# Optimization experiments

Measured on AMD Instinct MI355X. Metric: run time of the kernel, lower is better.

Reference implementation:

```python
import jax, jax.numpy as jnp
import numpy as np

N_MOLS = 2048       # number of molecules (segments)
BOND_FDIM = 14      # slice last BOND_FDIM columns of f_bonds
DEPTH = 3


def setup_inputs() -> dict:
    key = jax.random.key(0)
    ks = jax.random.split(key, 12)
    n_atoms, n_bonds = 65536, 131072
    atom_fdim, bond_total, hidden, max_nb = 133, 147, 256, 6
    atom_features = jax.random.normal(ks[0], (n_atoms, atom_fdim), jnp.float32)
    f_bonds = jax.random.normal(ks[1], (n_bonds, bond_total), jnp.float32)
    a2a = jax.random.randint(ks[2], (n_atoms, max_nb), 0, n_atoms, jnp.int32)
    a2b = jax.random.randint(ks[3], (n_atoms, max_nb), 0, n_bonds, jnp.int32)
    segment_ids = jnp.sort(jax.random.randint(ks[4], (n_atoms,), 0, N_MOLS, jnp.int32))
    s = 0.05
    Wi = jax.random.normal(ks[5], (atom_fdim, hidden), jnp.float32) * s
    bi = jax.random.normal(ks[6], (hidden,), jnp.float32) * s
    Wh = jax.random.normal(ks[7], (hidden + BOND_FDIM, hidden), jnp.float32) * s
    bh = jax.random.normal(ks[8], (hidden,), jnp.float32) * s
    Wo = jax.random.normal(ks[9], (atom_fdim + hidden, hidden), jnp.float32) * s
    bo = jax.random.normal(ks[10], (hidden,), jnp.float32) * s
    return {"atom_features": atom_features, "f_bonds": f_bonds, "a2a": a2a,
            "a2b": a2b, "segment_ids": segment_ids,
            "Wi": Wi, "bi": bi, "Wh": Wh, "bh": bh, "Wo": Wo, "bo": bo}


def reference(atom_features, f_bonds, a2a, a2b, segment_ids, Wi, bi, Wh, bh, Wo, bo):
    # W_i + ReLU
    inp = atom_features @ Wi + bi                      # [N, H]
    message = jax.nn.relu(inp)
    fb = f_bonds[:, -BOND_FDIM:]                       # slice last bond_fdim cols
    # depth-1 message passing steps
    for _ in range(DEPTH - 1):
        nei_a_sum = message[a2a].sum(axis=1)           # [N, H]   gather + sum
        nei_b_sum = fb[a2b].sum(axis=1)                # [N, Fb]  gather + sum
        # sum(concat) == concat(sums) over neighbor axis
        m = jnp.concatenate([nei_a_sum, nei_b_sum], axis=1) @ Wh + bh
        message = jax.nn.relu(inp + m)                 # dropout: eval mode (identity)
    # final atom readout
    a_message = message[a2a].sum(axis=1)               # [N, H]
    a_input = jnp.concatenate([atom_features, a_message], axis=1)
    atom_hiddens = jax.nn.relu(a_input @ Wo + bo)      # [N, H]
    # segment-mean pooling over molecules (empty segments -> zero vector)
    sums = jax.ops.segment_sum(atom_hiddens, segment_ids, num_segments=N_MOLS)
    counts = jax.ops.segment_sum(jnp.ones((atom_hiddens.shape[0],), atom_hiddens.dtype),
                                 segment_ids, num_segments=N_MOLS)
    vecs = jnp.where(counts[:, None] > 0, sums / jnp.maximum(counts, 1.0)[:, None], 0.0)
    return vecs
```

## Files before the change

kernel.cpp:

```cpp
#include <hip/hip_runtime.h>

#define N_ATOMS 65536
#define AF      133
#define BT      147
#define HID     256
#define NNB     6
#define NM      2048

#define KI   160
#define KB   32
#define KP   256
#define LSI  168
#define LSB  40
#define LSP  264

typedef __attribute__((ext_vector_type(8))) short short8;
typedef __attribute__((ext_vector_type(4))) float f32x4;

__device__ __forceinline__ unsigned short f2bf(float f) {
    unsigned u = __builtin_bit_cast(unsigned, f);
    u += 0x7fffu + ((u >> 16) & 1u);
    return (unsigned short)(u >> 16);
}
__device__ __forceinline__ float bf2f(unsigned short s) {
    unsigned u = ((unsigned)s) << 16;
    return __builtin_bit_cast(float, u);
}

__global__ __launch_bounds__(256) void k_prep_bond(const float* __restrict__ Wi,
                                                   const float* __restrict__ Wh,
                                                   const float* __restrict__ Wo,
                                                   const float* __restrict__ bi,
                                                   const float* __restrict__ bh,
                                                   const float* __restrict__ f_bonds,
                                                   const int* __restrict__ a2b,
                                                   unsigned short* __restrict__ Wi_t,
                                                   unsigned short* __restrict__ Wb_t,
                                                   unsigned short* __restrict__ Whm_t,
                                                   unsigned short* __restrict__ Woa_t,
                                                   unsigned short* __restrict__ Wom_t,
                                                   unsigned short* __restrict__ bondsum,
                                                   float* __restrict__ b_ih) {
    if (blockIdx.x < 256) {
        const int n = blockIdx.x;
        if (n == 0) b_ih[threadIdx.x] = bi[threadIdx.x] + bh[threadIdx.x];
        for (int k = threadIdx.x; k < KI; k += 256) {
            Wi_t[n * KI + k]  = f2bf(k < AF ? Wi[k * HID + n] : 0.f);
            Woa_t[n * KI + k] = f2bf(k < AF ? Wo[k * HID + n] : 0.f);
        }
        for (int k = threadIdx.x; k < KB; k += 256)
            Wb_t[n * KB + k] = f2bf(k < 14 ? Wh[(HID + k) * HID + n] : 0.f);
        for (int k = threadIdx.x; k < KP; k += 256) {
            Whm_t[n * KP + k] = f2bf(Wh[k * HID + n]);
            Wom_t[n * KP + k] = f2bf(Wo[(AF + k) * HID + n]);
        }
    } else {
        const int id   = (blockIdx.x - 256) * 256 + threadIdx.x;
        const int atom = id >> 4;
        const int c    = id & 15;
        float s = 0.f;
        if (c < 14) {
            const int* nb = &a2b[atom * NNB];
#pragma unroll
            for (int t = 0; t < NNB; ++t)
                s += f_bonds[(size_t)nb[t] * BT + (BT - 14) + c];
        }
        bondsum[atom * 32 + c]      = f2bf(s);
        bondsum[atom * 32 + 16 + c] = 0;
    }
}

template<int K, int LS>
__device__ __forceinline__ void mfma_core(const unsigned short* __restrict__ As,
                                          const unsigned short* __restrict__ Wt,
                                          f32x4 (&acc)[2][4], int wave, int lane) {
    const int lm = lane & 15, quad = lane >> 4;
    for (int ks = 0; ks < K; ks += 32) {
        short8 af[2], bf[4];
#pragma unroll
        for (int rt = 0; rt < 2; ++rt)
            af[rt] = *(const short8*)&As[(rt * 16 + lm) * LS + ks + quad * 8];
#pragma unroll
        for (int ct = 0; ct < 4; ++ct)
            bf[ct] = *(const short8*)&Wt[(size_t)(wave * 64 + ct * 16 + lm) * K + ks + quad * 8];
#pragma unroll
        for (int rt = 0; rt < 2; ++rt)
#pragma unroll
            for (int ct = 0; ct < 4; ++ct)
                acc[rt][ct] = __builtin_amdgcn_mfma_f32_16x16x32_bf16(af[rt], bf[ct], acc[rt][ct], 0, 0, 0);
    }
}

template<int K, int LS>
__device__ __forceinline__ void mfma_core2(const unsigned short* __restrict__ As,
                                           const unsigned short* __restrict__ WtA,
                                           const unsigned short* __restrict__ WtB,
                                           f32x4 (&accA)[2][4], f32x4 (&accB)[2][4],
                                           int wave, int lane) {
    const int lm = lane & 15, quad = lane >> 4;
    for (int ks = 0; ks < K; ks += 32) {
        short8 af[2], bfA[4], bfB[4];
#pragma unroll
        for (int rt = 0; rt < 2; ++rt)
            af[rt] = *(const short8*)&As[(rt * 16 + lm) * LS + ks + quad * 8];
#pragma unroll
        for (int ct = 0; ct < 4; ++ct) {
            size_t off = (size_t)(wave * 64 + ct * 16 + lm) * K + ks + quad * 8;
            bfA[ct] = *(const short8*)&WtA[off];
            bfB[ct] = *(const short8*)&WtB[off];
        }
#pragma unroll
        for (int rt = 0; rt < 2; ++rt)
#pragma unroll
            for (int ct = 0; ct < 4; ++ct) {
                accA[rt][ct] = __builtin_amdgcn_mfma_f32_16x16x32_bf16(af[rt], bfA[ct], accA[rt][ct], 0, 0, 0);
                accB[rt][ct] = __builtin_amdgcn_mfma_f32_16x16x32_bf16(af[rt], bfB[ct], accB[rt][ct], 0, 0, 0);
            }
    }
}

__device__ __forceinline__ void epi_to_lds(f32x4 (&acc)[2][4],
                                           const float* __restrict__ bias,
                                           bool relu_,
                                           unsigned short* __restrict__ E,
                                           int wave, int lane) {
    const int lm = lane & 15, quad = lane >> 4;
#pragma unroll
    for (int ct = 0; ct < 4; ++ct) {
        int col = wave * 64 + ct * 16 + lm;
        float bv = bias ? bias[col] : 0.f;
#pragma unroll
        for (int rt = 0; rt < 2; ++rt)
#pragma unroll
            for (int i = 0; i < 4; ++i) {
                float v = acc[rt][ct][i] + bv;
                if (relu_) v = fmaxf(v, 0.f);
                E[(rt * 16 + quad * 4 + i) * LSP + col] = f2bf(v);
            }
    }
}

__device__ __forceinline__ void store_tile32(unsigned short* __restrict__ dst, int base,
                                             const unsigned short* __restrict__ E, int tid) {
#pragma unroll
    for (int k = 0; k < 4; ++k) {
        int j = k * 256 + tid;
        int r = j >> 5, g = j & 31;
        *(short8*)&dst[(size_t)(base + r) * HID + g * 8] = *(const short8*)&E[r * LSP + g * 8];
    }
}

__global__ __launch_bounds__(256, 4) void k_inp(const float* __restrict__ atom,
                                                const unsigned short* __restrict__ bondsum,
                                                const unsigned short* __restrict__ Wi_t,
                                                const unsigned short* __restrict__ Wb_t,
                                                const unsigned short* __restrict__ Whm_t,
                                                const unsigned short* __restrict__ Woa_t,
                                                const float* __restrict__ bi,
                                                const float* __restrict__ b_ih,
                                                const float* __restrict__ bo,
                                                unsigned short* __restrict__ P0,
                                                unsigned short* __restrict__ inp2,
                                                unsigned short* __restrict__ aw) {
    __shared__ unsigned short atomT[32 * LSI];
    __shared__ unsigned short work[32 * LSP];
    __shared__ unsigned short bs[32 * LSB];
    const int tid  = threadIdx.x;
    const int base = blockIdx.x * 32;

    for (int it = tid; it < 32 * KI; it += 256) {
        int r = it / KI, c = it - r * KI;
        atomT[r * LSI + c] = f2bf(c < AF ? atom[(size_t)(base + r) * AF + c] : 0.f);
    }
    if (tid < 128) {
        int r = tid >> 2, c = (tid & 3) * 8;
        *(short8*)&bs[r * LSB + c] = *(const short8*)&bondsum[(size_t)(base + r) * 32 + c];
    }
    __syncthreads();

    const int lane = tid & 63, wave = tid >> 6;
    f32x4 acc1[2][4] = {}, acc3[2][4] = {};
    mfma_core2<KI, LSI>(atomT, Wi_t, Woa_t, acc1, acc3, wave, lane);

    epi_to_lds(acc3, bo, false, work, wave, lane);
    __syncthreads();
    store_tile32(aw, base, work, tid);
    __syncthreads();

    epi_to_lds(acc1, bi, true, work, wave, lane);
    __syncthreads();

    f32x4 acc2[2][4] = {};
    mfma_core<KP, LSP>(work, Whm_t, acc2, wave, lane);
    mfma_core<KB, LSB>(bs, Wb_t, acc1, wave, lane);
    __syncthreads();

    epi_to_lds(acc2, nullptr, false, work, wave, lane);
    __syncthreads();
    store_tile32(P0, base, work, tid);
    __syncthreads();
    epi_to_lds(acc1, b_ih, false, work, wave, lane);
    __syncthreads();
    store_tile32(inp2, base, work, tid);
}

__global__ __launch_bounds__(256, 6) void k_it(const unsigned short* __restrict__ Pin,
                                               const unsigned short* __restrict__ base_,
                                               const int* __restrict__ a2a,
                                               const unsigned short* __restrict__ Wt,
                                               unsigned short* __restrict__ Pout) {
    __shared__ unsigned short mT[32 * LSP];
    __shared__ int nb_l[32 * NNB];
    const int tid  = threadIdx.x;
    const int base = blockIdx.x * 32;

    if (tid < 32 * NNB) nb_l[tid] = a2a[base * NNB + tid];
    __syncthreads();

#pragma unroll 1
    for (int k = 0; k < 4; ++k) {
        int j = k * 256 + tid;
        int r = j >> 5, g = j & 31;
        const int* nb = &nb_l[r * NNB];
        float s[8] = {};
#pragma unroll
        for (int t = 0; t < NNB; ++t) {
            short8 u = *(const short8*)&Pin[(size_t)nb[t] * HID + g * 8];
#pragma unroll
            for (int q = 0; q < 8; ++q) s[q] += bf2f((unsigned short)u[q]);
        }
        short8 b = *(const short8*)&base_[(size_t)(base + r) * HID + g * 8];
        short8 o;
#pragma unroll
        for (int q = 0; q < 8; ++q)
            o[q] = (short)f2bf(fmaxf(s[q] + bf2f((unsigned short)b[q]), 0.f));
        *(short8*)&mT[r * LSP + g * 8] = o;
    }
    __syncthreads();

    const int lane = tid & 63, wave = tid >> 6;
    f32x4 acc[2][4] = {};
    mfma_core<KP, LSP>(mT, Wt, acc, wave, lane);
    __syncthreads();
    epi_to_lds(acc, nullptr, false, mT, wave, lane);
    __syncthreads();
    store_tile32(Pout, base, mT, tid);
}

__global__ __launch_bounds__(256, 6) void k_gseg(const unsigned short* __restrict__ P,
                                                 const unsigned short* __restrict__ aw,
                                                 const int* __restrict__ a2a,
                                                 const int* __restrict__ seg,
                                                 float* __restrict__ out) {
    const int m = blockIdx.x;
    __shared__ int lohi[2];
    __shared__ float red[8 * 256];
    if (threadIdx.x == 0) {
        int lo = 0, hi = N_ATOMS;
        while (lo < hi) { int mid = (lo + hi) >> 1; if (seg[mid] < m) lo = mid + 1; else hi = mid; }
        lohi[0] = lo;
        int lo2 = lo, hi2 = N_ATOMS;
        while (lo2 < hi2) { int mid = (lo2 + hi2) >> 1; if (seg[mid] < m + 1) lo2 = mid + 1; else hi2 = mid; }
        lohi[1] = lo2;
    }
    __syncthreads();
    const int lo = lohi[0], hi = lohi[1];
    const int slot = threadIdx.x >> 5;
    const int cg   = threadIdx.x & 31;

    float s[8] = {};
#pragma unroll 1
    for (int i0 = lo; i0 < hi; i0 += 8) {
        int i = i0 + slot;
        if (i < hi) {
            const int* nb = &a2a[i * NNB];
            short8 a = *(const short8*)&aw[(size_t)i * HID + cg * 8];
            float v[8];
#pragma unroll
            for (int q = 0; q < 8; ++q) v[q] = bf2f((unsigned short)a[q]);
#pragma unroll
            for (int t = 0; t < NNB; ++t) {
                short8 u = *(const short8*)&P[(size_t)nb[t] * HID + cg * 8];
#pragma unroll
                for (int q = 0; q < 8; ++q) v[q] += bf2f((unsigned short)u[q]);
            }
#pragma unroll
            for (int q = 0; q < 8; ++q) s[q] += fmaxf(v[q], 0.f);
        }
    }
#pragma unroll
    for (int q = 0; q < 8; ++q) red[slot * 256 + cg * 8 + q] = s[q];
    __syncthreads();

    const int j = threadIdx.x;
    float tot = 0.f;
#pragma unroll
    for (int sl = 0; sl < 8; ++sl) tot += red[sl * 256 + j];
    const int cnt = hi - lo;
    out[m * HID + j] = (cnt > 0) ? (tot / (float)cnt) : 0.f;
}

extern "C" void kernel_launch(void* const* d_in, const int* in_sizes, int n_in,
                              void* d_out, int out_size, void* d_ws, size_t ws_size,
                              hipStream_t stream) {
    const float* atom    = (const float*)d_in[0];
    const float* f_bonds = (const float*)d_in[1];
    const int*   a2a     = (const int*)d_in[2];
    const int*   a2b     = (const int*)d_in[3];
    const int*   seg     = (const int*)d_in[4];
    const float* Wi      = (const float*)d_in[5];
    const float* bi      = (const float*)d_in[6];
    const float* Wh      = (const float*)d_in[7];
    const float* bh      = (const float*)d_in[8];
    const float* Wo      = (const float*)d_in[9];
    const float* bo      = (const float*)d_in[10];
    float* out = (float*)d_out;

    unsigned short* ws = (unsigned short*)d_ws;
    const size_t nh = (size_t)N_ATOMS * HID;
    unsigned short* Pa   = ws;
    unsigned short* Pb   = Pa + nh;
    unsigned short* inp2 = Pb + nh;
    unsigned short* aw   = inp2 + nh;
    unsigned short* bsum = aw + nh;
    unsigned short* Wi_t  = bsum + (size_t)N_ATOMS * 32;
    unsigned short* Wb_t  = Wi_t + 256 * KI;
    unsigned short* Whm_t = Wb_t + 256 * KB;
    unsigned short* Woa_t = Whm_t + 256 * KP;
    unsigned short* Wom_t = Woa_t + 256 * KI;
    float*          b_ih  = (float*)(Wom_t + 256 * KP);

    dim3 blk(256);
    const int nb32 = N_ATOMS / 32;

    k_prep_bond<<<256 + N_ATOMS * 16 / 256, blk, 0, stream>>>(
        Wi, Wh, Wo, bi, bh, f_bonds, a2b,
        Wi_t, Wb_t, Whm_t, Woa_t, Wom_t, bsum, b_ih);
    k_inp<<<nb32, blk, 0, stream>>>(atom, bsum, Wi_t, Wb_t, Whm_t, Woa_t,
                                    bi, b_ih, bo, Pa, inp2, aw);

    k_it<<<nb32, blk, 0, stream>>>(Pa, inp2, a2a, Whm_t, Pb);
    k_it<<<nb32, blk, 0, stream>>>(Pb, inp2, a2a, Wom_t, Pa);
    k_gseg<<<NM, blk, 0, stream>>>(Pa, aw, a2a, seg, out);
}
```

Before: 374.7 us.

## Pre-swizzle weights into MFMA fragment order and reduce k_inp barriers

Weights are now written in an MFMA-fragment-ordered layout, so each lane loads its B fragment as one contiguous short8 and a wave reads fully coalesced 1KB chunks instead of strided rows. The K loops are fully unrolled. In k_inp the shared buffers are pooled so the atom tile buffer is reused as a second epilogue buffer, which lets two epilogues and two stores share one barrier and removes several __syncthreads. This costs extra index math in the prep kernel and more register pressure from unrolling.

Result: faster. 329.1 us (-12.2%).

```diff
diff --git a/kernel.cpp b/kernel.cpp
--- a/kernel.cpp
+++ b/kernel.cpp
@@ -25,6 +25,11 @@
 __device__ __forceinline__ float bf2f(unsigned short s) {
     unsigned u = ((unsigned)s) << 16;
     return __builtin_bit_cast(float, u);
+}
+
+__device__ __forceinline__ size_t fidx(int K, int n, int k) {
+    return ((size_t)(((n >> 4) * (K >> 5) + (k >> 5)) * 64
+                     + (((k >> 3) & 3) << 4) + (n & 15)) << 3) + (k & 7);
 }
 
 __global__ __launch_bounds__(256) void k_prep_bond(const float* __restrict__ Wi,
@@ -34,25 +39,25 @@
                                                    const float* __restrict__ bh,
                                                    const float* __restrict__ f_bonds,
                                                    const int* __restrict__ a2b,
-                                                   unsigned short* __restrict__ Wi_t,
-                                                   unsigned short* __restrict__ Wb_t,
-                                                   unsigned short* __restrict__ Whm_t,
-                                                   unsigned short* __restrict__ Woa_t,
-                                                   unsigned short* __restrict__ Wom_t,
+                                                   unsigned short* __restrict__ Wi_f,
+                                                   unsigned short* __restrict__ Wb_f,
+                                                   unsigned short* __restrict__ Whm_f,
+                                                   unsigned short* __restrict__ Woa_f,
+                                                   unsigned short* __restrict__ Wom_f,
                                                    unsigned short* __restrict__ bondsum,
                                                    float* __restrict__ b_ih) {
     if (blockIdx.x < 256) {
         const int n = blockIdx.x;
         if (n == 0) b_ih[threadIdx.x] = bi[threadIdx.x] + bh[threadIdx.x];
         for (int k = threadIdx.x; k < KI; k += 256) {
-            Wi_t[n * KI + k]  = f2bf(k < AF ? Wi[k * HID + n] : 0.f);
-            Woa_t[n * KI + k] = f2bf(k < AF ? Wo[k * HID + n] : 0.f);
+            Wi_f[fidx(KI, n, k)]  = f2bf(k < AF ? Wi[k * HID + n] : 0.f);
+            Woa_f[fidx(KI, n, k)] = f2bf(k < AF ? Wo[k * HID + n] : 0.f);
         }
         for (int k = threadIdx.x; k < KB; k += 256)
-            Wb_t[n * KB + k] = f2bf(k < 14 ? Wh[(HID + k) * HID + n] : 0.f);
+            Wb_f[fidx(KB, n, k)] = f2bf(k < 14 ? Wh[(HID + k) * HID + n] : 0.f);
         for (int k = threadIdx.x; k < KP; k += 256) {
-            Whm_t[n * KP + k] = f2bf(Wh[k * HID + n]);
-            Wom_t[n * KP + k] = f2bf(Wo[(AF + k) * HID + n]);
+            Whm_f[fidx(KP, n, k)] = f2bf(Wh[k * HID + n]);
+            Wom_f[fidx(KP, n, k)] = f2bf(Wo[(AF + k) * HID + n]);
         }
     } else {
         const int id   = (blockIdx.x - 256) * 256 + threadIdx.x;
@@ -75,14 +80,16 @@
                                           const unsigned short* __restrict__ Wt,
                                           f32x4 (&acc)[2][4], int wave, int lane) {
     const int lm = lane & 15, quad = lane >> 4;
-    for (int ks = 0; ks < K; ks += 32) {
+    const short8* __restrict__ Wf = (const short8*)Wt;
+#pragma unroll
+    for (int ks = 0; ks < (K >> 5); ++ks) {
         short8 af[2], bf[4];
 #pragma unroll
         for (int rt = 0; rt < 2; ++rt)
-            af[rt] = *(const short8*)&As[(rt * 16 + lm) * LS + ks + quad * 8];
+            af[rt] = *(const short8*)&As[(rt * 16 + lm) * LS + ks * 32 + quad * 8];
 #pragma unroll
         for (int ct = 0; ct < 4; ++ct)
-            bf[ct] = *(const short8*)&Wt[(size_t)(wave * 64 + ct * 16 + lm) * K + ks + quad * 8];
+            bf[ct] = Wf[(size_t)((wave * 4 + ct) * (K >> 5) + ks) * 64 + lane];
 #pragma unroll
         for (int rt = 0; rt < 2; ++rt)
 #pragma unroll
@@ -98,16 +105,19 @@
                                            f32x4 (&accA)[2][4], f32x4 (&accB)[2][4],
                                            int wave, int lane) {
     const int lm = lane & 15, quad = lane >> 4;
-    for (int ks = 0; ks < K; ks += 32) {
+    const short8* __restrict__ WfA = (const short8*)WtA;
+    const short8* __restrict__ WfB = (const short8*)WtB;
+#pragma unroll
+    for (int ks = 0; ks < (K >> 5); ++ks) {
         short8 af[2], bfA[4], bfB[4];
 #pragma unroll
         for (int rt = 0; rt < 2; ++rt)
-            af[rt] = *(const short8*)&As[(rt * 16 + lm) * LS + ks + quad * 8];
+            af[rt] = *(const short8*)&As[(rt * 16 + lm) * LS + ks * 32 + quad * 8];
 #pragma unroll
         for (int ct = 0; ct < 4; ++ct) {
-            size_t off = (size_t)(wave * 64 + ct * 16 + lm) * K + ks + quad * 8;
-            bfA[ct] = *(const short8*)&WtA[off];
-            bfB[ct] = *(const short8*)&WtB[off];
+            size_t off = (size_t)((wave * 4 + ct) * (K >> 5) + ks) * 64 + lane;
+            bfA[ct] = WfA[off];
+            bfB[ct] = WfB[off];
         }
 #pragma unroll
         for (int rt = 0; rt < 2; ++rt)
@@ -152,25 +162,26 @@
 
 __global__ __launch_bounds__(256, 4) void k_inp(const float* __restrict__ atom,
                                                 const unsigned short* __restrict__ bondsum,
-                                                const unsigned short* __restrict__ Wi_t,
-                                                const unsigned short* __restrict__ Wb_t,
-                                                const unsigned short* __restrict__ Whm_t,
-                                                const unsigned short* __restrict__ Woa_t,
+                                                const unsigned short* __restrict__ Wi_f,
+                                                const unsigned short* __restrict__ Wb_f,
+                                                const unsigned short* __restrict__ Whm_f,
+                                                const unsigned short* __restrict__ Woa_f,
                                                 const float* __restrict__ bi,
                                                 const float* __restrict__ b_ih,
                                                 const float* __restrict__ bo,
                                                 unsigned short* __restrict__ P0,
                                                 unsigned short* __restrict__ inp2,
                                                 unsigned short* __restrict__ aw) {
-    __shared__ unsigned short atomT[32 * LSI];
-    __shared__ unsigned short work[32 * LSP];
-    __shared__ unsigned short bs[32 * LSB];
+    __shared__ unsigned short pool[8448 + 8448 + 1280];
+    unsigned short* X    = pool;
+    unsigned short* work = pool + 8448;
+    unsigned short* bs   = pool + 16896;
     const int tid  = threadIdx.x;
     const int base = blockIdx.x * 32;
 
     for (int it = tid; it < 32 * KI; it += 256) {
         int r = it / KI, c = it - r * KI;
-        atomT[r * LSI + c] = f2bf(c < AF ? atom[(size_t)(base + r) * AF + c] : 0.f);
+        X[r * LSI + c] = f2bf(c < AF ? atom[(size_t)(base + r) * AF + c] : 0.f);
     }
     if (tid < 128) {
         int r = tid >> 2, c = (tid & 3) * 8;
@@ -180,27 +191,24 @@
 
     const int lane = tid & 63, wave = tid >> 6;
     f32x4 acc1[2][4] = {}, acc3[2][4] = {};
-    mfma_core2<KI, LSI>(atomT, Wi_t, Woa_t, acc1, acc3, wave, lane);
-
-    epi_to_lds(acc3, bo, false, work, wave, lane);
-    __syncthreads();
-    store_tile32(aw, base, work, tid);
-    __syncthreads();
-
+    mfma_core2<KI, LSI>(X, Wi_f, Woa_f, acc1, acc3, wave, lane);
+    __syncthreads();
+
+    epi_to_lds(acc3, bo, false, X, wave, lane);
     epi_to_lds(acc1, bi, true, work, wave, lane);
     __syncthreads();
 
+    store_tile32(aw, base, X, tid);
     f32x4 acc2[2][4] = {};
-    mfma_core<KP, LSP>(work, Whm_t, acc2, wave, lane);
-    mfma_core<KB, LSB>(bs, Wb_t, acc1, wave, lane);
-    __syncthreads();
-
-    epi_to_lds(acc2, nullptr, false, work, wave, lane);
-    __syncthreads();
-    store_tile32(P0, base, work, tid);
-    __syncthreads();
+    mfma_core<KP, LSP>(work, Whm_f, acc2, wave, lane);
+    mfma_core<KB, LSB>(bs, Wb_f, acc1, wave, lane);
+    __syncthreads();
+
+    epi_to_lds(acc2, nullptr, false, X, wave, lane);
     epi_to_lds(acc1, b_ih, false, work, wave, lane);
     __syncthreads();
+
+    store_tile32(P0, base, X, tid);
     store_tile32(inp2, base, work, tid);
 }
 
@@ -323,23 +331,23 @@
     unsigned short* inp2 = Pb + nh;
     unsigned short* aw   = inp2 + nh;
     unsigned short* bsum = aw + nh;
-    unsigned short* Wi_t  = bsum + (size_t)N_ATOMS * 32;
-    unsigned short* Wb_t  = Wi_t + 256 * KI;
-    unsigned short* Whm_t = Wb_t + 256 * KB;
-    unsigned short* Woa_t = Whm_t + 256 * KP;
-    unsigned short* Wom_t = Woa_t + 256 * KI;
-    float*          b_ih  = (float*)(Wom_t + 256 * KP);
+    unsigned short* Wi_f  = bsum + (size_t)N_ATOMS * 32;
+    unsigned short* Wb_f  = Wi_f + 256 * KI;
+    unsigned short* Whm_f = Wb_f + 256 * KB;
+    unsigned short* Woa_f = Whm_f + 256 * KP;
+    unsigned short* Wom_f = Woa_f + 256 * KI;
+    float*          b_ih  = (float*)(Wom_f + 256 * KP);
 
     dim3 blk(256);
     const int nb32 = N_ATOMS / 32;
 
     k_prep_bond<<<256 + N_ATOMS * 16 / 256, blk, 0, stream>>>(
         Wi, Wh, Wo, bi, bh, f_bonds, a2b,
-        Wi_t, Wb_t, Whm_t, Woa_t, Wom_t, bsum, b_ih);
-    k_inp<<<nb32, blk, 0, stream>>>(atom, bsum, Wi_t, Wb_t, Whm_t, Woa_t,
+        Wi_f, Wb_f, Whm_f, Woa_f, Wom_f, bsum, b_ih);
+    k_inp<<<nb32, blk, 0, stream>>>(atom, bsum, Wi_f, Wb_f, Whm_f, Woa_f,
                                     bi, b_ih, bo, Pa, inp2, aw);
 
-    k_it<<<nb32, blk, 0, stream>>>(Pa, inp2, a2a, Whm_t, Pb);
-    k_it<<<nb32, blk, 0, stream>>>(Pb, inp2, a2a, Wom_t, Pa);
+    k_it<<<nb32, blk, 0, stream>>>(Pa, inp2, a2a, Whm_f, Pb);
+    k_it<<<nb32, blk, 0, stream>>>(Pb, inp2, a2a, Wom_f, Pa);
     k_gseg<<<NM, blk, 0, stream>>>(Pa, aw, a2a, seg, out);
 }
```
